# Optimization experiments

Measured on AMD Instinct MI355X. Metric: run time of the kernel, lower is better.

## Reference

```python
import jax, jax.numpy as jnp
import numpy as np

N = 16384
E = 262144

def _deg_norm(idx, n):
    deg = jax.ops.segment_sum(jnp.ones((idx.shape[0],), jnp.float32), idx, num_segments=n)
    return jnp.where(deg > 0, deg ** -0.5, 0.0)  # DGL norm='both' with zero-in-degree allowed

def _graph_conv(x, W, b, edge_src, edge_dst, c_src, c_dst):
    # DGL GraphConv(norm='both'): h = D_in^{-1/2} A D_out^{-1/2} (x W) + b
    h = (x * c_src[:, None]) @ W            # [N, out] (mult-first order; linear, so equivalent)
    msg = h[edge_src]                        # gather over edges [E, out]
    agg = jax.ops.segment_sum(msg, edge_dst, num_segments=x.shape[0])
    return agg * c_dst[:, None] + b

def setup_inputs() -> dict:
    key = jax.random.key(0)
    ks = jax.random.split(key, 8)
    return {
        "features": jax.random.normal(ks[0], (N, 256), jnp.float32),
        "W1": jax.random.normal(ks[1], (256, 128), jnp.float32) * 0.05,
        "b1": jnp.zeros((128,), jnp.float32),
        "Wm": jax.random.normal(ks[2], (128, 64), jnp.float32) * 0.05,
        "bm": jnp.zeros((64,), jnp.float32),
        "Ws": jax.random.normal(ks[3], (128, 64), jnp.float32) * 0.05,
        "bs": jnp.zeros((64,), jnp.float32),
        "noise": jax.random.normal(ks[4], (N, 64), jnp.float32),
        "edge_src": jax.random.randint(ks[5], (E,), 0, N, jnp.int32),
        "edge_dst": jax.random.randint(ks[6], (E,), 0, N, jnp.int32),
    }

def reference(features, W1, b1, Wm, bm, Ws, bs, noise, edge_src, edge_dst):
    n = features.shape[0]
    c_src = _deg_norm(edge_src, n)   # out-degree norm
    c_dst = _deg_norm(edge_dst, n)   # in-degree norm
    h = jax.nn.relu(_graph_conv(features, W1, b1, edge_src, edge_dst, c_src, c_dst))
    mean = _graph_conv(h, Wm, bm, edge_src, edge_dst, c_src, c_dst)
    log_std = _graph_conv(h, Ws, bs, edge_src, edge_dst, c_src, c_dst)
    z = mean + noise * jnp.exp(log_std)      # reparameterization
    # InnerProductDecoder with act=identity (dropout inactive at eval), then sigmoid
    pre = jax.nn.sigmoid(z @ z.T)            # [N, N]
    return (pre, z)
```

## Files before the change

kernel.cpp:

```cpp
#include <hip/hip_runtime.h>
#include <hip/hip_bf16.h>


typedef short short8 __attribute__((ext_vector_type(8)));
typedef float f32x4 __attribute__((ext_vector_type(4)));

__global__ void k_deg(const int* __restrict__ src, const int* __restrict__ dst,
                      float* __restrict__ cs, float* __restrict__ cd, int E) {
  int i = blockIdx.x * blockDim.x + threadIdx.x;
  if (i < E) {
    atomicAdd(&cs[src[i]], 1.0f);
    atomicAdd(&cd[dst[i]], 1.0f);
  }
}

__global__ void __launch_bounds__(256) k_scan(const float* __restrict__ cnt,
                                              int* __restrict__ off, int n) {
  __shared__ int sums[256];
  const int t = threadIdx.x;
  const int per = n / 256;
  const int base = t * per;
  int s = 0;
  for (int i = 0; i < per; ++i) s += (int)cnt[base + i];
  sums[t] = s;
  __syncthreads();
  for (int d = 1; d < 256; d <<= 1) {
    int v = (t >= d) ? sums[t - d] : 0;
    __syncthreads();
    sums[t] += v;
    __syncthreads();
  }
  int run = t ? sums[t - 1] : 0;
  for (int i = 0; i < per; ++i) { off[base + i] = run; run += (int)cnt[base + i]; }
  if (t == 255) off[n] = run;
}

__global__ void k_cnorm(float* __restrict__ cs, float* __restrict__ cd, int n) {
  int i = blockIdx.x * blockDim.x + threadIdx.x;
  if (i < n) {
    float a = cs[i]; cs[i] = (a > 0.f) ? rsqrtf(a) : 0.f;
    float b = cd[i]; cd[i] = (b > 0.f) ? rsqrtf(b) : 0.f;
  }
}

__global__ void k_fill(const int* __restrict__ src, const int* __restrict__ dst,
                       const int* __restrict__ off, int* __restrict__ cursor,
                       int* __restrict__ elist, int E) {
  int e = blockIdx.x * blockDim.x + threadIdx.x;
  if (e < E) {
    int d = dst[e];
    int pos = atomicAdd(&cursor[d], 1);
    elist[off[d] + pos] = src[e];
  }
}

__global__ void __launch_bounds__(128) k_xw1(const float* __restrict__ x,
                                             const float* __restrict__ W,
                                             const float* __restrict__ cs,
                                             float* __restrict__ out) {
  __shared__ float xs[8][256];
  const int rb = blockIdx.x * 8;
  const int t = threadIdx.x;
#pragma unroll
  for (int r = 0; r < 8; ++r) {
    float c = cs[rb + r];
    xs[r][t]       = x[(size_t)(rb + r) * 256 + t] * c;
    xs[r][t + 128] = x[(size_t)(rb + r) * 256 + t + 128] * c;
  }
  __syncthreads();
  float acc[8] = {};
  for (int k = 0; k < 256; ++k) {
    float w = W[k * 128 + t];
#pragma unroll
    for (int r = 0; r < 8; ++r) acc[r] += xs[r][k] * w;
  }
#pragma unroll
  for (int r = 0; r < 8; ++r) out[(size_t)(rb + r) * 128 + t] = acc[r];
}

__global__ void __launch_bounds__(256) k_gather1(const float* __restrict__ tmp,
                                                 const int* __restrict__ off,
                                                 const int* __restrict__ elist,
                                                 const float* __restrict__ cd,
                                                 const float* __restrict__ cs,
                                                 const float* __restrict__ b,
                                                 float* __restrict__ hs) {
  const int node = blockIdx.x * 4 + (threadIdx.x >> 6);
  const int lane = threadIdx.x & 63;
  const int half = lane >> 5;
  const int c4 = (lane & 31) << 2;
  const int e0 = off[node], e1 = off[node + 1];
  f32x4 a = {0.f, 0.f, 0.f, 0.f};
  for (int e = e0 + half; e < e1; e += 2)
    a += *reinterpret_cast<const f32x4*>(tmp + (size_t)elist[e] * 128 + c4);
  a.x += __shfl_xor(a.x, 32);
  a.y += __shfl_xor(a.y, 32);
  a.z += __shfl_xor(a.z, 32);
  a.w += __shfl_xor(a.w, 32);
  if (half == 0) {
    const float c = cd[node], s = cs[node];
    f32x4 bb = *reinterpret_cast<const f32x4*>(b + c4);
    f32x4 r;
    r.x = fmaxf(a.x * c + bb.x, 0.f) * s;
    r.y = fmaxf(a.y * c + bb.y, 0.f) * s;
    r.z = fmaxf(a.z * c + bb.z, 0.f) * s;
    r.w = fmaxf(a.w * c + bb.w, 0.f) * s;
    *reinterpret_cast<f32x4*>(hs + (size_t)node * 128 + c4) = r;
  }
}

__global__ void __launch_bounds__(256) k_gather2(const float* __restrict__ hs,
                                                 const int* __restrict__ off,
                                                 const int* __restrict__ elist,
                                                 const float* __restrict__ cd,
                                                 float* __restrict__ s2c) {
  const int node = blockIdx.x * 4 + (threadIdx.x >> 6);
  const int lane = threadIdx.x & 63;
  const int half = lane >> 5;
  const int c4 = (lane & 31) << 2;
  const int e0 = off[node], e1 = off[node + 1];
  f32x4 a = {0.f, 0.f, 0.f, 0.f};
  for (int e = e0 + half; e < e1; e += 2)
    a += *reinterpret_cast<const f32x4*>(hs + (size_t)elist[e] * 128 + c4);
  a.x += __shfl_xor(a.x, 32);
  a.y += __shfl_xor(a.y, 32);
  a.z += __shfl_xor(a.z, 32);
  a.w += __shfl_xor(a.w, 32);
  if (half == 0) {
    const float c = cd[node];
    *reinterpret_cast<f32x4*>(s2c + (size_t)node * 128 + c4) = a * c;
  }
}

__global__ void __launch_bounds__(128) k_zfin(const float* __restrict__ s2c,
                                              const float* __restrict__ Wm,
                                              const float* __restrict__ Ws,
                                              const float* __restrict__ bm,
                                              const float* __restrict__ bs,
                                              const float* __restrict__ noise,
                                              float* __restrict__ z,
                                              __hip_bfloat16* __restrict__ zb) {
  __shared__ float xs[8][128];
  __shared__ float ys[8][128];
  const int rb = blockIdx.x * 8;
  const int t = threadIdx.x;
#pragma unroll
  for (int r = 0; r < 8; ++r) xs[r][t] = s2c[(size_t)(rb + r) * 128 + t];
  __syncthreads();
  const float* W = (t < 64) ? Wm : Ws;
  const float bias = (t < 64) ? bm[t & 63] : bs[t & 63];
  const int col = t & 63;
  float acc[8] = {};
  for (int k = 0; k < 128; ++k) {
    float w = W[k * 64 + col];
#pragma unroll
    for (int r = 0; r < 8; ++r) acc[r] += xs[r][k] * w;
  }
#pragma unroll
  for (int r = 0; r < 8; ++r) ys[r][t] = acc[r] + bias;
  __syncthreads();
#pragma unroll
  for (int q = 0; q < 4; ++q) {
    int idx = t + 128 * q;
    int row = idx >> 6, c = idx & 63;
    float zv = ys[row][c] + noise[(size_t)(rb + row) * 64 + c] * __expf(ys[row][c + 64]);
    z[(size_t)(rb + row) * 64 + c]  = zv;
    zb[(size_t)(rb + row) * 64 + c] = __float2bfloat16(zv);
  }
}

__global__ void __launch_bounds__(256) k_zz_mfma(const short* __restrict__ zb,
                                                 float* __restrict__ pre, int n) {
  const int wave = threadIdx.x >> 6, lane = threadIdx.x & 63;
  const int wr = wave >> 1, wc = wave & 1;
  const int brow = blockIdx.y * 128 + wr * 64;
  const int bcol = blockIdx.x * 128 + wc * 64;
  const int lrow = lane & 15;
  const int kq = lane >> 4;

  short8 afrag[2][4], bfrag[2][4];
#pragma unroll
  for (int tt = 0; tt < 4; ++tt) {
#pragma unroll
    for (int ks = 0; ks < 2; ++ks) {
      afrag[ks][tt] = *reinterpret_cast<const short8*>(
          zb + (size_t)(brow + tt * 16 + lrow) * 64 + ks * 32 + kq * 8);
      bfrag[ks][tt] = *reinterpret_cast<const short8*>(
          zb + (size_t)(bcol + tt * 16 + lrow) * 64 + ks * 32 + kq * 8);
    }
  }

  f32x4 acc[4][4];
#pragma unroll
  for (int i = 0; i < 4; ++i)
#pragma unroll
    for (int j = 0; j < 4; ++j) acc[i][j] = (f32x4){0.f, 0.f, 0.f, 0.f};

#pragma unroll
  for (int i = 0; i < 4; ++i)
#pragma unroll
    for (int j = 0; j < 4; ++j) {
      acc[i][j] = __builtin_amdgcn_mfma_f32_16x16x32_bf16(afrag[0][i], bfrag[0][j], acc[i][j], 0, 0, 0);
      acc[i][j] = __builtin_amdgcn_mfma_f32_16x16x32_bf16(afrag[1][i], bfrag[1][j], acc[i][j], 0, 0, 0);
    }

  const int crow0 = kq * 4;
#pragma unroll
  for (int i = 0; i < 4; ++i) {
#pragma unroll
    for (int r = 0; r < 4; ++r) {
      size_t rowoff = (size_t)(brow + i * 16 + crow0 + r) * (size_t)n;
#pragma unroll
      for (int j = 0; j < 4; ++j) {
        float v = acc[i][j][r];
        pre[rowoff + bcol + j * 16 + lrow] = 1.f / (1.f + __expf(-v));
      }
    }
  }
}

extern "C" void kernel_launch(void* const* d_in, const int* in_sizes, int n_in,
                              void* d_out, int out_size, void* d_ws, size_t ws_size,
                              hipStream_t stream) {
  const float* feat  = (const float*)d_in[0];
  const float* W1    = (const float*)d_in[1];
  const float* b1    = (const float*)d_in[2];
  const float* Wm    = (const float*)d_in[3];
  const float* bm    = (const float*)d_in[4];
  const float* Ws    = (const float*)d_in[5];
  const float* bs    = (const float*)d_in[6];
  const float* noise = (const float*)d_in[7];
  const int* esrc    = (const int*)d_in[8];
  const int* edst    = (const int*)d_in[9];

  const int N = in_sizes[0] / 256;
  const int E = in_sizes[8];

  float* out = (float*)d_out;
  float* z   = out + (size_t)N * N;

  char* ws = (char*)d_ws;
  float* c_src  = (float*)(ws + 0);
  float* c_dst  = (float*)(ws + 65536);
  int*   cursor = (int*)  (ws + 131072);
  int*   off    = (int*)  (ws + 196608);
  int*   elist  = (int*)  (ws + 327680);
  float* bufA   = (float*)(ws + 2097152);
  float* hs     = (float*)(ws + 10485760);
  __hip_bfloat16* zb = (__hip_bfloat16*)(ws + 18874368);

  hipMemsetAsync(ws, 0, 196608, stream);
  k_deg<<<(E + 255) / 256, 256, 0, stream>>>(esrc, edst, c_src, c_dst, E);
  k_scan<<<1, 256, 0, stream>>>(c_dst, off, N);
  k_cnorm<<<(N + 255) / 256, 256, 0, stream>>>(c_src, c_dst, N);
  k_fill<<<(E + 255) / 256, 256, 0, stream>>>(esrc, edst, off, cursor, elist, E);

  k_xw1<<<N / 8, 128, 0, stream>>>(feat, W1, c_src, bufA);
  k_gather1<<<N / 4, 256, 0, stream>>>(bufA, off, elist, c_dst, c_src, b1, hs);

  k_gather2<<<N / 4, 256, 0, stream>>>(hs, off, elist, c_dst, bufA);
  k_zfin<<<N / 8, 128, 0, stream>>>(bufA, Wm, Ws, bm, bs, noise, z, zb);

  dim3 zgrid(N / 128, N / 128);
  k_zz_mfma<<<zgrid, 256, 0, stream>>>((const short*)zb, out, N);
}
```

Measured before the change: 430.0 us.

## Use split-bf16 MFMA for both dense encoder matmuls with pretransposed weights

Replaces the scalar fp32 FMA kernels for X·W1 and the fused mean/log_std projection with MFMA bf16 kernels. Each fp32 value is split into hi and lo bf16 parts, and three MFMAs per tile product keep accuracy close to fp32. Weights are transposed and split once per call by two small prep kernels. This offloads the dense GEMMs to matrix cores, at the cost of extra conversion ALU work, two added launches, and a larger LDS buffer in the epilogue.

```diff
diff --git a/kernel.cpp b/kernel.cpp
--- a/kernel.cpp
+++ b/kernel.cpp
@@ -54,28 +54,96 @@
   }
 }
 
-__global__ void __launch_bounds__(128) k_xw1(const float* __restrict__ x,
-                                             const float* __restrict__ W,
-                                             const float* __restrict__ cs,
-                                             float* __restrict__ out) {
-  __shared__ float xs[8][256];
-  const int rb = blockIdx.x * 8;
-  const int t = threadIdx.x;
-#pragma unroll
-  for (int r = 0; r < 8; ++r) {
-    float c = cs[rb + r];
-    xs[r][t]       = x[(size_t)(rb + r) * 256 + t] * c;
-    xs[r][t + 128] = x[(size_t)(rb + r) * 256 + t + 128] * c;
-  }
-  __syncthreads();
-  float acc[8] = {};
-  for (int k = 0; k < 256; ++k) {
-    float w = W[k * 128 + t];
-#pragma unroll
-    for (int r = 0; r < 8; ++r) acc[r] += xs[r][k] * w;
-  }
-#pragma unroll
-  for (int r = 0; r < 8; ++r) out[(size_t)(rb + r) * 128 + t] = acc[r];
+__global__ void k_wprep1(const float* __restrict__ W, short* __restrict__ hi,
+                         short* __restrict__ lo) {
+  int idx = blockIdx.x * 256 + threadIdx.x;
+  int c = idx >> 8, k = idx & 255;
+  float v = W[k * 128 + c];
+  __hip_bfloat16 hb = __float2bfloat16(v);
+  float hf = __bfloat162float(hb);
+  __hip_bfloat16 lb = __float2bfloat16(v - hf);
+  hi[c * 256 + k] = *reinterpret_cast<short*>(&hb);
+  lo[c * 256 + k] = *reinterpret_cast<short*>(&lb);
+}
+
+__global__ void k_wprep2(const float* __restrict__ Wm, const float* __restrict__ Ws,
+                         short* __restrict__ hi, short* __restrict__ lo) {
+  int idx = blockIdx.x * 256 + threadIdx.x;
+  int c = idx >> 7, k = idx & 127;
+  float v = (c < 64) ? Wm[k * 64 + c] : Ws[k * 64 + (c - 64)];
+  __hip_bfloat16 hb = __float2bfloat16(v);
+  float hf = __bfloat162float(hb);
+  __hip_bfloat16 lb = __float2bfloat16(v - hf);
+  hi[c * 128 + k] = *reinterpret_cast<short*>(&hb);
+  lo[c * 128 + k] = *reinterpret_cast<short*>(&lb);
+}
+
+__global__ void __launch_bounds__(256) k_enc1(const float* __restrict__ x,
+                                              const short* __restrict__ wt_hi,
+                                              const short* __restrict__ wt_lo,
+                                              const float* __restrict__ cs,
+                                              float* __restrict__ out) {
+  const int wave = threadIdx.x >> 6, lane = threadIdx.x & 63;
+  const int lrow = lane & 15, kq = lane >> 4;
+  const int brow = blockIdx.x * 64;
+  const int bcol = wave * 32;
+
+  f32x4 acc[4][2];
+#pragma unroll
+  for (int i = 0; i < 4; ++i)
+#pragma unroll
+    for (int j = 0; j < 2; ++j) acc[i][j] = (f32x4){0.f, 0.f, 0.f, 0.f};
+
+  float crow[4];
+#pragma unroll
+  for (int i = 0; i < 4; ++i) crow[i] = cs[brow + i * 16 + lrow];
+
+  for (int ks = 0; ks < 8; ++ks) {
+    short8 ahi[4], alo[4];
+#pragma unroll
+    for (int i = 0; i < 4; ++i) {
+      const float* ap = x + (size_t)(brow + i * 16 + lrow) * 256 + ks * 32 + kq * 8;
+      f32x4 a0 = *reinterpret_cast<const f32x4*>(ap);
+      f32x4 a1 = *reinterpret_cast<const f32x4*>(ap + 4);
+      const float c = crow[i];
+      float vals[8] = {a0.x, a0.y, a0.z, a0.w, a1.x, a1.y, a1.z, a1.w};
+      short8 h, l;
+#pragma unroll
+      for (int j = 0; j < 8; ++j) {
+        float v = vals[j] * c;
+        __hip_bfloat16 hb = __float2bfloat16(v);
+        float hf = __bfloat162float(hb);
+        __hip_bfloat16 lb = __float2bfloat16(v - hf);
+        h[j] = *reinterpret_cast<short*>(&hb);
+        l[j] = *reinterpret_cast<short*>(&lb);
+      }
+      ahi[i] = h; alo[i] = l;
+    }
+    short8 bhi[2], blo[2];
+#pragma unroll
+    for (int j = 0; j < 2; ++j) {
+      size_t boff = (size_t)(bcol + j * 16 + lrow) * 256 + ks * 32 + kq * 8;
+      bhi[j] = *reinterpret_cast<const short8*>(wt_hi + boff);
+      blo[j] = *reinterpret_cast<const short8*>(wt_lo + boff);
+    }
+#pragma unroll
+    for (int i = 0; i < 4; ++i)
+#pragma unroll
+      for (int j = 0; j < 2; ++j) {
+        acc[i][j] = __builtin_amdgcn_mfma_f32_16x16x32_bf16(ahi[i], bhi[j], acc[i][j], 0, 0, 0);
+        acc[i][j] = __builtin_amdgcn_mfma_f32_16x16x32_bf16(ahi[i], blo[j], acc[i][j], 0, 0, 0);
+        acc[i][j] = __builtin_amdgcn_mfma_f32_16x16x32_bf16(alo[i], bhi[j], acc[i][j], 0, 0, 0);
+      }
+  }
+#pragma unroll
+  for (int i = 0; i < 4; ++i)
+#pragma unroll
+    for (int r = 0; r < 4; ++r) {
+      int row = brow + i * 16 + kq * 4 + r;
+#pragma unroll
+      for (int j = 0; j < 2; ++j)
+        out[(size_t)row * 128 + bcol + j * 16 + lrow] = acc[i][j][r];
+    }
 }
 
 __global__ void __launch_bounds__(256) k_gather1(const float* __restrict__ tmp,
@@ -132,40 +200,82 @@
   }
 }
 
-__global__ void __launch_bounds__(128) k_zfin(const float* __restrict__ s2c,
-                                              const float* __restrict__ Wm,
-                                              const float* __restrict__ Ws,
-                                              const float* __restrict__ bm,
-                                              const float* __restrict__ bs,
-                                              const float* __restrict__ noise,
-                                              float* __restrict__ z,
-                                              __hip_bfloat16* __restrict__ zb) {
-  __shared__ float xs[8][128];
-  __shared__ float ys[8][128];
-  const int rb = blockIdx.x * 8;
+__global__ void __launch_bounds__(256) k_zfin2(const float* __restrict__ s2c,
+                                               const short* __restrict__ wt_hi,
+                                               const short* __restrict__ wt_lo,
+                                               const float* __restrict__ bm,
+                                               const float* __restrict__ bs,
+                                               const float* __restrict__ noise,
+                                               float* __restrict__ z,
+                                               __hip_bfloat16* __restrict__ zb) {
+  __shared__ float ys[64][128];
+  const int wave = threadIdx.x >> 6, lane = threadIdx.x & 63;
+  const int lrow = lane & 15, kq = lane >> 4;
+  const int brow = blockIdx.x * 64;
+  const int bcol = wave * 32;
+
+  f32x4 acc[4][2];
+#pragma unroll
+  for (int i = 0; i < 4; ++i)
+#pragma unroll
+    for (int j = 0; j < 2; ++j) acc[i][j] = (f32x4){0.f, 0.f, 0.f, 0.f};
+
+  for (int ks = 0; ks < 4; ++ks) {
+    short8 ahi[4], alo[4];
+#pragma unroll
+    for (int i = 0; i < 4; ++i) {
+      const float* ap = s2c + (size_t)(brow + i * 16 + lrow) * 128 + ks * 32 + kq * 8;
+      f32x4 a0 = *reinterpret_cast<const f32x4*>(ap);
+      f32x4 a1 = *reinterpret_cast<const f32x4*>(ap + 4);
+      float vals[8] = {a0.x, a0.y, a0.z, a0.w, a1.x, a1.y, a1.z, a1.w};
+      short8 h, l;
+#pragma unroll
+      for (int j = 0; j < 8; ++j) {
+        float v = vals[j];
+        __hip_bfloat16 hb = __float2bfloat16(v);
+        float hf = __bfloat162float(hb);
+        __hip_bfloat16 lb = __float2bfloat16(v - hf);
+        h[j] = *reinterpret_cast<short*>(&hb);
+        l[j] = *reinterpret_cast<short*>(&lb);
+      }
+      ahi[i] = h; alo[i] = l;
+    }
+    short8 bhi[2], blo[2];
+#pragma unroll
+    for (int j = 0; j < 2; ++j) {
+      size_t boff = (size_t)(bcol + j * 16 + lrow) * 128 + ks * 32 + kq * 8;
+      bhi[j] = *reinterpret_cast<const short8*>(wt_hi + boff);
+      blo[j] = *reinterpret_cast<const short8*>(wt_lo + boff);
+    }
+#pragma unroll
+    for (int i = 0; i < 4; ++i)
+#pragma unroll
+      for (int j = 0; j < 2; ++j) {
+        acc[i][j] = __builtin_amdgcn_mfma_f32_16x16x32_bf16(ahi[i], bhi[j], acc[i][j], 0, 0, 0);
+        acc[i][j] = __builtin_amdgcn_mfma_f32_16x16x32_bf16(ahi[i], blo[j], acc[i][j], 0, 0, 0);
+        acc[i][j] = __builtin_amdgcn_mfma_f32_16x16x32_bf16(alo[i], bhi[j], acc[i][j], 0, 0, 0);
+      }
+  }
+#pragma unroll
+  for (int j = 0; j < 2; ++j) {
+    const int col = bcol + j * 16 + lrow;
+    const float bias = (col < 64) ? bm[col] : bs[col - 64];
+#pragma unroll
+    for (int i = 0; i < 4; ++i)
+#pragma unroll
+      for (int r = 0; r < 4; ++r)
+        ys[i * 16 + kq * 4 + r][col] = acc[i][j][r] + bias;
+  }
+  __syncthreads();
   const int t = threadIdx.x;
 #pragma unroll
-  for (int r = 0; r < 8; ++r) xs[r][t] = s2c[(size_t)(rb + r) * 128 + t];
-  __syncthreads();
-  const float* W = (t < 64) ? Wm : Ws;
-  const float bias = (t < 64) ? bm[t & 63] : bs[t & 63];
-  const int col = t & 63;
-  float acc[8] = {};
-  for (int k = 0; k < 128; ++k) {
-    float w = W[k * 64 + col];
-#pragma unroll
-    for (int r = 0; r < 8; ++r) acc[r] += xs[r][k] * w;
-  }
-#pragma unroll
-  for (int r = 0; r < 8; ++r) ys[r][t] = acc[r] + bias;
-  __syncthreads();
-#pragma unroll
-  for (int q = 0; q < 4; ++q) {
-    int idx = t + 128 * q;
+  for (int q = 0; q < 16; ++q) {
+    int idx = t + 256 * q;
     int row = idx >> 6, c = idx & 63;
-    float zv = ys[row][c] + noise[(size_t)(rb + row) * 64 + c] * __expf(ys[row][c + 64]);
-    z[(size_t)(rb + row) * 64 + c]  = zv;
-    zb[(size_t)(rb + row) * 64 + c] = __float2bfloat16(zv);
+    float m = ys[row][c], ls = ys[row][c + 64];
+    float zv = m + noise[(size_t)(brow + row) * 64 + c] * __expf(ls);
+    z[(size_t)(brow + row) * 64 + c]  = zv;
+    zb[(size_t)(brow + row) * 64 + c] = __float2bfloat16(zv);
   }
 }
 
@@ -245,9 +355,16 @@
   int*   cursor = (int*)  (ws + 131072);
   int*   off    = (int*)  (ws + 196608);
   int*   elist  = (int*)  (ws + 327680);
+  short* w1t_hi = (short*)(ws + 1376256);
+  short* w1t_lo = (short*)(ws + 1441792);
+  short* w2t_hi = (short*)(ws + 1507328);
+  short* w2t_lo = (short*)(ws + 1540096);
   float* bufA   = (float*)(ws + 2097152);
   float* hs     = (float*)(ws + 10485760);
   __hip_bfloat16* zb = (__hip_bfloat16*)(ws + 18874368);
+
+  k_wprep1<<<128, 256, 0, stream>>>(W1, w1t_hi, w1t_lo);
+  k_wprep2<<<64, 256, 0, stream>>>(Wm, Ws, w2t_hi, w2t_lo);
 
   hipMemsetAsync(ws, 0, 196608, stream);
   k_deg<<<(E + 255) / 256, 256, 0, stream>>>(esrc, edst, c_src, c_dst, E);
@@ -255,11 +372,11 @@
   k_cnorm<<<(N + 255) / 256, 256, 0, stream>>>(c_src, c_dst, N);
   k_fill<<<(E + 255) / 256, 256, 0, stream>>>(esrc, edst, off, cursor, elist, E);
 
-  k_xw1<<<N / 8, 128, 0, stream>>>(feat, W1, c_src, bufA);
+  k_enc1<<<N / 64, 256, 0, stream>>>(feat, w1t_hi, w1t_lo, c_src, bufA);
   k_gather1<<<N / 4, 256, 0, stream>>>(bufA, off, elist, c_dst, c_src, b1, hs);
 
   k_gather2<<<N / 4, 256, 0, stream>>>(hs, off, elist, c_dst, bufA);
-  k_zfin<<<N / 8, 128, 0, stream>>>(bufA, Wm, Ws, bm, bs, noise, z, zb);
+  k_zfin2<<<N / 64, 256, 0, stream>>>(bufA, w2t_hi, w2t_lo, bm, bs, noise, z, zb);
 
   dim3 zgrid(N / 128, N / 128);
   k_zz_mfma<<<zgrid, 256, 0, stream>>>((const short*)zb, out, N);
```

Measured after the change: 408.8 us. -4.9%, faster.
